# Kernel optimization log

Hardware: AMD Instinct MI355X
Metric: run time of the kernel (lower is better)

Reference implementation:

```python
import jax, jax.numpy as jnp
import numpy as np

N = 100000   # nodes
E = 600000   # edges
G = 4096     # graphs in batch
D_IN = 73
D_E = 101
D = 128      # latent_dim
BN_EPS = 1e-5


def _bn(h, gamma, beta):
    # BatchNorm1d in training mode: batch statistics (biased variance)
    m = h.mean(axis=0)
    v = h.var(axis=0)
    return (h - m) * jax.lax.rsqrt(v + BN_EPS) * gamma + beta


def setup_inputs() -> dict:
    key = jax.random.key(0)
    ks = jax.random.split(key, 24)
    inp = {
        "x": jax.random.normal(ks[0], (N, D_IN), jnp.float32),
        "edge_attr": jax.random.normal(ks[1], (E, D_E), jnp.float32),
        "src": jax.random.randint(ks[2], (E,), 0, N, jnp.int32),
        "dst": jax.random.randint(ks[3], (E,), 0, N, jnp.int32),
        "batch": jnp.sort(jax.random.randint(ks[4], (N,), 0, G, jnp.int32)),
        # node embedding Linear(73 -> 128)
        "W_emb": jax.random.normal(ks[5], (D_IN, D), jnp.float32) / np.sqrt(D_IN),
        "b_emb": jnp.zeros((D,), jnp.float32),
    }
    k = 6
    for i in range(2):
        inp[f"We{i}"] = jax.random.normal(ks[k], (D_E, D), jnp.float32) / np.sqrt(D_E); k += 1
        inp[f"be{i}"] = jnp.zeros((D,), jnp.float32)
        inp[f"W1_{i}"] = jax.random.normal(ks[k], (D, 2 * D), jnp.float32) / np.sqrt(D); k += 1
        inp[f"b1_{i}"] = jnp.zeros((2 * D,), jnp.float32)
        inp[f"g1_{i}"] = jnp.ones((2 * D,), jnp.float32)
        inp[f"bb1_{i}"] = jnp.zeros((2 * D,), jnp.float32)
        inp[f"W2_{i}"] = jax.random.normal(ks[k], (2 * D, D), jnp.float32) / np.sqrt(2 * D); k += 1
        inp[f"b2_{i}"] = jnp.zeros((D,), jnp.float32)
        inp[f"go_{i}"] = jnp.ones((D,), jnp.float32)
        inp[f"bo_{i}"] = jnp.zeros((D,), jnp.float32)
    return inp


def _forward(x, edge_attr, src, dst, batch,
             W_emb, b_emb,
             We0, be0, W1_0, b1_0, g1_0, bb1_0, W2_0, b2_0, go_0, bo_0,
             We1, be1, W1_1, b1_1, g1_1, bb1_1, W2_1, b2_1, go_1, bo_1):
    layers = [
        (We0, be0, W1_0, b1_0, g1_0, bb1_0, W2_0, b2_0, go_0, bo_0),
        (We1, be1, W1_1, b1_1, g1_1, bb1_1, W2_1, b2_1, go_1, bo_1),
    ]
    h = x @ W_emb + b_emb  # [N, D]
    n_layers = len(layers)
    for i, (We, be, W1, b1, g1, bb1, W2, b2, go, bo) in enumerate(layers):
        e = edge_attr @ We + be                         # [E, D]
        msg = jax.nn.relu(h[src] + e)                   # gather + add + ReLU
        agg = jax.ops.segment_sum(msg, dst, num_segments=N)  # scatter-sum
        z = h + agg                                     # (1 + eps) * x_i + aggr, eps = 0
        z = jax.nn.relu(_bn(z @ W1 + b1, g1, bb1))      # MLP: Linear -> BN -> ReLU
        h = _bn(z @ W2 + b2, go, bo)                    # Linear -> outer BN
        if i != n_layers - 1:
            h = jax.nn.relu(h)
        # dropout p=0 -> identity
    # global mean pool over graphs
    sums = jax.ops.segment_sum(h, batch, num_segments=G)            # [G, D]
    counts = jax.ops.segment_sum(jnp.ones((h.shape[0],), h.dtype), batch, num_segments=G)
    return sums / jnp.maximum(counts, 1.0)[:, None]


def reference(x, edge_attr, src, dst, batch,
              W_emb, b_emb,
              We0, be0, W1_0, b1_0, g1_0, bb1_0, W2_0, b2_0, go_0, bo_0,
              We1, be1, W1_1, b1_1, g1_1, bb1_1, W2_1, b2_1, go_1, bo_1):
    return _forward(x, edge_attr, src, dst, batch, W_emb, b_emb,
                    We0, be0, W1_0, b1_0, g1_0, bb1_0, W2_0, b2_0, go_0, bo_0,
                    We1, be1, W1_1, b1_1, g1_1, bb1_1, W2_1, b2_1, go_1, bo_1)
```

## Files before the change

kernel.cpp:

```cpp
#include <hip/hip_runtime.h>
#include <cstddef>

#define NN  100000
#define NE  600000
#define NG  4096
#define DIN 73
#define DE  101
#define DD  128
#define DD2 256
#define NP  100096
#define EP  600064

typedef unsigned int uint;
typedef unsigned short ushort;
typedef __attribute__((ext_vector_type(8))) short bf16x8;
typedef __attribute__((ext_vector_type(4))) float f32x4;

__device__ __forceinline__ void fadd_atomic(float* p, float v) { unsafeAtomicAdd(p, v); }

__device__ __forceinline__ ushort f2bf(float f) {
    uint u = __float_as_uint(f);
    uint r = (u + 0x7fffu + ((u >> 16) & 1u)) >> 16;
    return (ushort)r;
}
__device__ __forceinline__ float bf2f(ushort u) { return __uint_as_float(((uint)u) << 16); }


__global__ void hist_kernel(const int* __restrict__ dst, int* __restrict__ deg) {
    int e = blockIdx.x * blockDim.x + threadIdx.x;
    if (e < NE) atomicAdd(&deg[dst[e]], 1);
}

__global__ __launch_bounds__(256) void scan_chunk_kernel(
    const int* __restrict__ deg, int* __restrict__ offs, int* __restrict__ csums)
{
    const int b = blockIdx.x, t = threadIdx.x;
    const int base = b * 1024 + t * 4;
    int v[4];
    #pragma unroll
    for (int i = 0; i < 4; ++i) v[i] = (base + i < NN) ? deg[base + i] : 0;
    int tsum = v[0] + v[1] + v[2] + v[3];
    const int lane = t & 63, w = t >> 6;
    int x = tsum;
    #pragma unroll
    for (int d = 1; d < 64; d <<= 1) {
        int y = __shfl_up(x, d, 64);
        if (lane >= d) x += y;
    }
    __shared__ int wsum[4];
    if (lane == 63) wsum[w] = x;
    __syncthreads();
    int woff = 0;
    for (int i = 0; i < w; ++i) woff += wsum[i];
    int run = woff + x - tsum;
    #pragma unroll
    for (int i = 0; i < 4; ++i) {
        if (base + i < NN) offs[base + i] = run;
        run += v[i];
    }
    if (t == 255) csums[b] = woff + x;
}

__global__ void scan_tops_kernel(int* __restrict__ csums, int* __restrict__ offs, int nchunks) {
    if (threadIdx.x == 0 && blockIdx.x == 0) {
        int run = 0;
        for (int i = 0; i < nchunks; ++i) { int c = csums[i]; csums[i] = run; run += c; }
        offs[NN] = run;
    }
}

__global__ void scan_add_kernel(int* __restrict__ offs, const int* __restrict__ csums) {
    int i = blockIdx.x * blockDim.x + threadIdx.x;
    if (i < NN) offs[i] += csums[i >> 10];
}

__global__ void scatter_kernel(const int* __restrict__ dst, const int* __restrict__ src,
                               const int* __restrict__ offs, int* __restrict__ cursor,
                               int* __restrict__ eperm, int* __restrict__ srcp)
{
    int e = blockIdx.x * blockDim.x + threadIdx.x;
    if (e >= NE) return;
    int d = dst[e];
    int pos = offs[d] + atomicAdd(&cursor[d], 1);
    eperm[e] = pos;
    srcp[pos] = src[e];
}

__global__ void gstart_kernel(const int* __restrict__ batch, int* __restrict__ gstart) {
    int n = blockIdx.x * blockDim.x + threadIdx.x;
    if (n > NN) return;
    if (n == NN) {
        for (int g = batch[NN - 1] + 1; g <= NG; ++g) gstart[g] = NN;
        return;
    }
    int b = batch[n];
    int pb = (n == 0) ? -1 : batch[n - 1];
    for (int g = pb + 1; g <= b; ++g) gstart[g] = n;
}


__global__ __launch_bounds__(256) void cvt_ea_kernel(const float* __restrict__ ea,
                                                     ushort* __restrict__ eab)
{
    const int t = threadIdx.x;
    const int r = blockIdx.x * 8 + (t >> 5);
    if (r >= EP) return;
    const int c = (t & 31) * 4;
    ushort4 o = {0, 0, 0, 0};
    if (r < NE) {
        o.x = (c + 0 < DE) ? f2bf(ea[(size_t)r * DE + c + 0]) : (ushort)0;
        o.y = (c + 1 < DE) ? f2bf(ea[(size_t)r * DE + c + 1]) : (ushort)0;
        o.z = (c + 2 < DE) ? f2bf(ea[(size_t)r * DE + c + 2]) : (ushort)0;
        o.w = (c + 3 < DE) ? f2bf(ea[(size_t)r * DE + c + 3]) : (ushort)0;
    }
    *(ushort4*)&eab[(size_t)r * 128 + c] = o;
}

__global__ void cvt_wt_kernel(const float* __restrict__ in, ushort* __restrict__ out,
                              int Kin, int Nn, int Kp)
{
    const int n = blockIdx.x;
    for (int k = threadIdx.x; k < Kp; k += blockDim.x)
        out[(size_t)n * Kp + k] = (k < Kin) ? f2bf(in[(size_t)k * Nn + n]) : (ushort)0;
}

template<int K>
__device__ __forceinline__ void mma_core(const ushort* __restrict__ Wt,
                                         const ushort* __restrict__ X,
                                         int n0, int m0, f32x4 acc[4][8])
{
    const int lane = threadIdx.x & 63;
    const int l15 = lane & 15, grp = lane >> 4;
    const size_t aoff = (size_t)(n0 + l15) * K + grp * 8;
    const size_t boff = (size_t)(m0 + l15) * K + grp * 8;
    #pragma unroll
    for (int kk = 0; kk < K / 32; ++kk) {
        bf16x8 a[8], b[4];
        #pragma unroll
        for (int nf = 0; nf < 8; ++nf)
            a[nf] = *(const bf16x8*)(Wt + aoff + (size_t)nf * 16 * K + kk * 32);
        #pragma unroll
        for (int mf = 0; mf < 4; ++mf)
            b[mf] = *(const bf16x8*)(X + boff + (size_t)mf * 16 * K + kk * 32);
        #pragma unroll
        for (int mf = 0; mf < 4; ++mf)
            #pragma unroll
            for (int nf = 0; nf < 8; ++nf)
                acc[mf][nf] = __builtin_amdgcn_mfma_f32_16x16x32_bf16(a[nf], b[mf], acc[mf][nf], 0, 0, 0);
    }
}

__device__ __forceinline__ void acc_zero(f32x4 acc[4][8]) {
    #pragma unroll
    for (int i = 0; i < 4; ++i)
        #pragma unroll
        for (int j = 0; j < 8; ++j)
            acc[i][j] = (f32x4){0.f, 0.f, 0.f, 0.f};
}

__global__ __launch_bounds__(256) void edge_gemm_kernel(
    const ushort* __restrict__ eab, const ushort* __restrict__ Wt,
    const float* __restrict__ be, const int* __restrict__ eperm,
    ushort* __restrict__ ecsr)
{
    const int e0 = blockIdx.x * 256 + (threadIdx.x >> 6) * 64;
    const int lane = threadIdx.x & 63, l15 = lane & 15, grp = lane >> 4;
    int pos[4];
    #pragma unroll
    for (int mf = 0; mf < 4; ++mf) {
        const int e = e0 + mf * 16 + l15;
        pos[mf] = (e < NE) ? eperm[e] : -1;
    }
    f32x4 acc[4][8];
    acc_zero(acc);
    mma_core<128>(Wt, eab, 0, e0, acc);
    float4 bev[8];
    #pragma unroll
    for (int nf = 0; nf < 8; ++nf) bev[nf] = *(const float4*)&be[nf * 16 + grp * 4];
    #pragma unroll
    for (int mf = 0; mf < 4; ++mf) {
        if (pos[mf] < 0) continue;
        ushort* rp = &ecsr[(size_t)pos[mf] * 128];
        #pragma unroll
        for (int nf = 0; nf < 8; ++nf) {
            const int nb = nf * 16 + grp * 4;
            ushort4 o;
            o.x = f2bf(acc[mf][nf][0] + bev[nf].x);
            o.y = f2bf(acc[mf][nf][1] + bev[nf].y);
            o.z = f2bf(acc[mf][nf][2] + bev[nf].z);
            o.w = f2bf(acc[mf][nf][3] + bev[nf].w);
            *(ushort4*)&rp[nb] = o;
        }
    }
}

__global__ __launch_bounds__(256) void agg_kernel(
    const int* __restrict__ offs, const int* __restrict__ srcp,
    const ushort* __restrict__ ecsr, const ushort* __restrict__ hb,
    ushort* __restrict__ zb)
{
    const int n = blockIdx.x * 4 + (threadIdx.x >> 6);
    if (n >= NN) return;
    const int lane = threadIdx.x & 63;
    const int s = offs[n], t = offs[n + 1];
    float a0 = 0.f, a1 = 0.f;
    for (int i = s; i < t; ++i) {
        const int sp = srcp[i];
        const uint ev = *(const uint*)&ecsr[(size_t)i * 128 + lane * 2];
        const uint hv = *(const uint*)&hb[(size_t)sp * 128 + lane * 2];
        a0 += fmaxf(__uint_as_float(ev << 16) + __uint_as_float(hv << 16), 0.f);
        a1 += fmaxf(__uint_as_float(ev & 0xffff0000u) + __uint_as_float(hv & 0xffff0000u), 0.f);
    }
    const uint hh = *(const uint*)&hb[(size_t)n * 128 + lane * 2];
    ushort2 o;
    o.x = f2bf(__uint_as_float(hh << 16) + a0);
    o.y = f2bf(__uint_as_float(hh & 0xffff0000u) + a1);
    *(ushort2*)&zb[(size_t)n * 128 + lane * 2] = o;
}

__global__ __launch_bounds__(256) void mlp1_gemm_kernel(
    const ushort* __restrict__ z, const ushort* __restrict__ Wt,
    const float* __restrict__ bias, ushort* __restrict__ y)
{
    f32x4 acc[4][8];
    acc_zero(acc);
    const int m0 = blockIdx.x * 256 + (threadIdx.x >> 6) * 64;
    const int n0 = blockIdx.y * 128;
    mma_core<128>(Wt, z, n0, m0, acc);
    const int lane = threadIdx.x & 63, l15 = lane & 15, grp = lane >> 4;
    #pragma unroll
    for (int nf = 0; nf < 8; ++nf) {
        const int nb = n0 + nf * 16 + grp * 4;
        const float4 bv = *(const float4*)&bias[nb];
        #pragma unroll
        for (int mf = 0; mf < 4; ++mf) {
            const size_t m = m0 + mf * 16 + l15;
            ushort4 o;
            o.x = f2bf(acc[mf][nf][0] + bv.x);
            o.y = f2bf(acc[mf][nf][1] + bv.y);
            o.z = f2bf(acc[mf][nf][2] + bv.z);
            o.w = f2bf(acc[mf][nf][3] + bv.w);
            *(ushort4*)&y[m * 256 + nb] = o;
        }
    }
}

__global__ __launch_bounds__(256) void mlp2_gemm_kernel(
    const ushort* __restrict__ y1, const ushort* __restrict__ Wt,
    const float* __restrict__ bias, ushort* __restrict__ y2)
{
    f32x4 acc[4][8];
    acc_zero(acc);
    const int m0 = blockIdx.x * 256 + (threadIdx.x >> 6) * 64;
    mma_core<256>(Wt, y1, 0, m0, acc);
    const int lane = threadIdx.x & 63, l15 = lane & 15, grp = lane >> 4;
    #pragma unroll
    for (int nf = 0; nf < 8; ++nf) {
        const int nb = nf * 16 + grp * 4;
        const float4 bv = *(const float4*)&bias[nb];
        #pragma unroll
        for (int mf = 0; mf < 4; ++mf) {
            const size_t m = m0 + mf * 16 + l15;
            ushort4 o;
            o.x = f2bf(acc[mf][nf][0] + bv.x);
            o.y = f2bf(acc[mf][nf][1] + bv.y);
            o.z = f2bf(acc[mf][nf][2] + bv.z);
            o.w = f2bf(acc[mf][nf][3] + bv.w);
            *(ushort4*)&y2[m * 128 + nb] = o;
        }
    }
}


__global__ __launch_bounds__(128) void embed_kernel(
    const float* __restrict__ x, const float* __restrict__ W,
    const float* __restrict__ b, ushort* __restrict__ hb)
{
    __shared__ float xs[4][DIN];
    const int n0 = blockIdx.x * 4;
    const int d  = threadIdx.x;
    for (int idx = d; idx < 4 * DIN; idx += 128) {
        int r = idx / DIN, c = idx - r * DIN;
        xs[r][c] = x[(size_t)n0 * DIN + idx];
    }
    __syncthreads();
    float bb = b[d];
    float a0 = bb, a1 = bb, a2 = bb, a3 = bb;
    for (int k = 0; k < DIN; ++k) {
        float w = W[k * DD + d];
        a0 = fmaf(xs[0][k], w, a0);
        a1 = fmaf(xs[1][k], w, a1);
        a2 = fmaf(xs[2][k], w, a2);
        a3 = fmaf(xs[3][k], w, a3);
    }
    hb[(size_t)(n0 + 0) * DD + d] = f2bf(a0);
    hb[(size_t)(n0 + 1) * DD + d] = f2bf(a1);
    hb[(size_t)(n0 + 2) * DD + d] = f2bf(a2);
    hb[(size_t)(n0 + 3) * DD + d] = f2bf(a3);
}

__global__ __launch_bounds__(256) void colstats256_kernel(
    const ushort* __restrict__ y, float* __restrict__ s, float* __restrict__ q)
{
    const int t = threadIdx.x;
    const int cs = (t & 63) * 4, rg = t >> 6;
    const int r0 = blockIdx.x * 256;
    float ps0 = 0, ps1 = 0, ps2 = 0, ps3 = 0, pq0 = 0, pq1 = 0, pq2 = 0, pq3 = 0;
    for (int i = rg; i < 256; i += 4) {
        const int r = r0 + i;
        if (r >= NN) break;
        ushort4 u = *(const ushort4*)&y[(size_t)r * 256 + cs];
        float f0 = bf2f(u.x), f1 = bf2f(u.y), f2v = bf2f(u.z), f3 = bf2f(u.w);
        ps0 += f0; pq0 += f0 * f0;
        ps1 += f1; pq1 += f1 * f1;
        ps2 += f2v; pq2 += f2v * f2v;
        ps3 += f3; pq3 += f3 * f3;
    }
    __shared__ float SS[4][256], SQ[4][256];
    SS[rg][cs + 0] = ps0; SS[rg][cs + 1] = ps1; SS[rg][cs + 2] = ps2; SS[rg][cs + 3] = ps3;
    SQ[rg][cs + 0] = pq0; SQ[rg][cs + 1] = pq1; SQ[rg][cs + 2] = pq2; SQ[rg][cs + 3] = pq3;
    __syncthreads();
    if (rg == 0) {
        #pragma unroll
        for (int j = 0; j < 4; ++j) {
            const int c = cs + j;
            fadd_atomic(&s[c], SS[0][c] + SS[1][c] + SS[2][c] + SS[3][c]);
            fadd_atomic(&q[c], SQ[0][c] + SQ[1][c] + SQ[2][c] + SQ[3][c]);
        }
    }
}

__global__ __launch_bounds__(256) void colstats128b_kernel(
    const ushort* __restrict__ y, float* __restrict__ s, float* __restrict__ q)
{
    const int t = threadIdx.x;
    const int cs = (t & 31) * 4, rg = t >> 5;
    const int r0 = blockIdx.x * 256;
    float ps0 = 0, ps1 = 0, ps2 = 0, ps3 = 0, pq0 = 0, pq1 = 0, pq2 = 0, pq3 = 0;
    for (int i = rg; i < 256; i += 8) {
        const int r = r0 + i;
        if (r >= NN) break;
        ushort4 u = *(const ushort4*)&y[(size_t)r * 128 + cs];
        float f0 = bf2f(u.x), f1 = bf2f(u.y), f2v = bf2f(u.z), f3 = bf2f(u.w);
        ps0 += f0; pq0 += f0 * f0;
        ps1 += f1; pq1 += f1 * f1;
        ps2 += f2v; pq2 += f2v * f2v;
        ps3 += f3; pq3 += f3 * f3;
    }
    __shared__ float SS[8][128], SQ[8][128];
    SS[rg][cs + 0] = ps0; SS[rg][cs + 1] = ps1; SS[rg][cs + 2] = ps2; SS[rg][cs + 3] = ps3;
    SQ[rg][cs + 0] = pq0; SQ[rg][cs + 1] = pq1; SQ[rg][cs + 2] = pq2; SQ[rg][cs + 3] = pq3;
    __syncthreads();
    if (rg == 0) {
        #pragma unroll
        for (int j = 0; j < 4; ++j) {
            const int c = cs + j;
            float sv = 0, qv = 0;
            #pragma unroll
            for (int g = 0; g < 8; ++g) { sv += SS[g][c]; qv += SQ[g][c]; }
            fadd_atomic(&s[c], sv);
            fadd_atomic(&q[c], qv);
        }
    }
}

__global__ void finalize_kernel(const float* __restrict__ s, const float* __restrict__ sq,
                                const float* __restrict__ g, const float* __restrict__ bb,
                                float* __restrict__ a, float* __restrict__ c,
                                int dim, float invN)
{
    int d = blockIdx.x * blockDim.x + threadIdx.x;
    if (d >= dim) return;
    float m  = s[d] * invN;
    float v  = sq[d] * invN - m * m;
    float rs = rsqrtf(v + 1e-5f);
    float ai = g[d] * rs;
    a[d] = ai;
    c[d] = bb[d] - m * ai;
}

__global__ void bnrelu_bf_kernel(ushort* __restrict__ y, const float* __restrict__ a,
                                 const float* __restrict__ c)
{
    int i = blockIdx.x * blockDim.x + threadIdx.x;
    const int stride = gridDim.x * blockDim.x;
    for (; i < NN * 64; i += stride) {
        const int cb = (i & 63) * 4;
        ushort4 u = *(const ushort4*)&y[(size_t)i * 4];
        const float4 av = *(const float4*)&a[cb];
        const float4 cv = *(const float4*)&c[cb];
        ushort4 o;
        o.x = f2bf(fmaxf(fmaf(bf2f(u.x), av.x, cv.x), 0.f));
        o.y = f2bf(fmaxf(fmaf(bf2f(u.y), av.y, cv.y), 0.f));
        o.z = f2bf(fmaxf(fmaf(bf2f(u.z), av.z, cv.z), 0.f));
        o.w = f2bf(fmaxf(fmaf(bf2f(u.w), av.w, cv.w), 0.f));
        *(ushort4*)&y[(size_t)i * 4] = o;
    }
}

__global__ void bnrelu_hb_kernel(ushort* __restrict__ hb, const float* __restrict__ a,
                                 const float* __restrict__ c)
{
    int i = blockIdx.x * blockDim.x + threadIdx.x;
    const int stride = gridDim.x * blockDim.x;
    for (; i < NN * 32; i += stride) {
        const int cb = (i & 31) * 4;
        ushort4 u = *(const ushort4*)&hb[(size_t)i * 4];
        const float4 av = *(const float4*)&a[cb];
        const float4 cv = *(const float4*)&c[cb];
        ushort4 o;
        o.x = f2bf(fmaxf(fmaf(bf2f(u.x), av.x, cv.x), 0.f));
        o.y = f2bf(fmaxf(fmaf(bf2f(u.y), av.y, cv.y), 0.f));
        o.z = f2bf(fmaxf(fmaf(bf2f(u.z), av.z, cv.z), 0.f));
        o.w = f2bf(fmaxf(fmaf(bf2f(u.w), av.w, cv.w), 0.f));
        *(ushort4*)&hb[(size_t)i * 4] = o;
    }
}

__global__ __launch_bounds__(256) void pool_kernel(
    const ushort* __restrict__ hb, const float* __restrict__ a2, const float* __restrict__ c2,
    const int* __restrict__ gstart, float* __restrict__ out)
{
    const int g = blockIdx.x * 4 + (threadIdx.x >> 6);
    if (g >= NG) return;
    const int lane = threadIdx.x & 63;
    const int s = gstart[g], t = gstart[g + 1];
    float a0 = 0.f, a1 = 0.f;
    for (int n = s; n < t; ++n) {
        const uint v = *(const uint*)&hb[(size_t)n * 128 + lane * 2];
        a0 += __uint_as_float(v << 16);
        a1 += __uint_as_float(v & 0xffff0000u);
    }
    const int d0 = lane * 2;
    float2 o;
    if (t > s) {
        const float inv = 1.0f / (float)(t - s);
        o.x = fmaf(a2[d0 + 0], a0 * inv, c2[d0 + 0]);
        o.y = fmaf(a2[d0 + 1], a1 * inv, c2[d0 + 1]);
    } else {
        o.x = 0.f; o.y = 0.f;
    }
    *(float2*)&out[(size_t)g * 128 + d0] = o;
}


extern "C" void kernel_launch(void* const* d_in, const int* in_sizes, int n_in,
                              void* d_out, int out_size, void* d_ws, size_t ws_size,
                              hipStream_t stream)
{
    (void)in_sizes; (void)n_in; (void)out_size; (void)ws_size;
    const float* x     = (const float*)d_in[0];
    const float* ea    = (const float*)d_in[1];
    const int*   src   = (const int*)d_in[2];
    const int*   dst   = (const int*)d_in[3];
    const int*   batch = (const int*)d_in[4];
    const float* W_emb = (const float*)d_in[5];
    const float* b_emb = (const float*)d_in[6];

    char* ws = (char*)d_ws;
    auto alloc = [&](size_t bytes) { void* p = ws; ws += (bytes + 255) & ~(size_t)255; return p; };

    ushort* hb  = (ushort*)alloc((size_t)NP * 128 * 2);
    ushort* zb  = (ushort*)alloc((size_t)NP * 128 * 2);
    ushort* eab = (ushort*)alloc((size_t)EP * 128 * 2);
    ushort* big = (ushort*)alloc((size_t)EP * 128 * 2);
    ushort* ecsr = big;
    ushort* y1b  = big;
    int* deg    = (int*)alloc((size_t)NN * 4);
    int* offs   = (int*)alloc((size_t)(NN + 1) * 4);
    int* eperm  = (int*)alloc((size_t)NE * 4);
    int* srcp   = (int*)alloc((size_t)NE * 4);
    int* csums  = (int*)alloc(128 * 4);
    int* gstart = (int*)alloc((size_t)(NG + 1) * 4);
    ushort* Wet[2], *W1t[2], *W2t[2];
    for (int l = 0; l < 2; ++l) {
        Wet[l] = (ushort*)alloc(128 * 128 * 2);
        W1t[l] = (ushort*)alloc(256 * 128 * 2);
        W2t[l] = (ushort*)alloc(128 * 256 * 2);
    }
    float* st = (float*)alloc(2048 * 4);
    float* s1 = st,        *sq1 = st + 256, *a1 = st + 512,  *c1 = st + 768;
    float* s2 = st + 1024, *sq2 = st + 1152, *a2 = st + 1280, *c2 = st + 1408;
    float* out = (float*)d_out;

    const int NCHUNK = (NN + 1023) / 1024;

    hipMemsetAsync(deg, 0, (size_t)NN * 4, stream);
    hist_kernel<<<(NE + 255) / 256, 256, 0, stream>>>(dst, deg);
    scan_chunk_kernel<<<NCHUNK, 256, 0, stream>>>(deg, offs, csums);
    scan_tops_kernel<<<1, 1, 0, stream>>>(csums, offs, NCHUNK);
    scan_add_kernel<<<(NN + 255) / 256, 256, 0, stream>>>(offs, csums);
    hipMemsetAsync(deg, 0, (size_t)NN * 4, stream);
    scatter_kernel<<<(NE + 255) / 256, 256, 0, stream>>>(dst, src, offs, deg, eperm, srcp);
    gstart_kernel<<<(NN + 256) / 256, 256, 0, stream>>>(batch, gstart);

    cvt_ea_kernel<<<EP / 8, 256, 0, stream>>>(ea, eab);
    for (int l = 0; l < 2; ++l) {
        const float* const* L = (const float* const*)(d_in + 7 + l * 10);
        cvt_wt_kernel<<<128, 128, 0, stream>>>(L[0], Wet[l], 101, 128, 128);
        cvt_wt_kernel<<<256, 128, 0, stream>>>(L[2], W1t[l], 128, 256, 128);
        cvt_wt_kernel<<<128, 128, 0, stream>>>(L[6], W2t[l], 256, 128, 256);
    }

    embed_kernel<<<NN / 4, 128, 0, stream>>>(x, W_emb, b_emb, hb);

    for (int layer = 0; layer < 2; ++layer) {
        const float* const* L = (const float* const*)(d_in + 7 + layer * 10);
        const float* be  = L[1];
        const float* b1  = L[3];
        const float* g1  = L[4]; const float* bb1 = L[5];
        const float* b2  = L[7];
        const float* go  = L[8]; const float* bo  = L[9];

        edge_gemm_kernel<<<EP / 256, 256, 0, stream>>>(eab, Wet[layer], be, eperm, ecsr);
        agg_kernel<<<NN / 4, 256, 0, stream>>>(offs, srcp, ecsr, hb, zb);

        hipMemsetAsync(s1, 0, 512 * sizeof(float), stream);
        hipMemsetAsync(s2, 0, 256 * sizeof(float), stream);

        mlp1_gemm_kernel<<<dim3(NP / 256, 2), 256, 0, stream>>>(zb, W1t[layer], b1, y1b);
        colstats256_kernel<<<NP / 256, 256, 0, stream>>>(y1b, s1, sq1);
        finalize_kernel<<<1, 256, 0, stream>>>(s1, sq1, g1, bb1, a1, c1, 256, 1.0f / NN);
        bnrelu_bf_kernel<<<2048, 256, 0, stream>>>(y1b, a1, c1);
        mlp2_gemm_kernel<<<NP / 256, 256, 0, stream>>>(y1b, W2t[layer], b2, hb);
        colstats128b_kernel<<<NP / 256, 256, 0, stream>>>(hb, s2, sq2);
        finalize_kernel<<<1, 128, 0, stream>>>(s2, sq2, go, bo, a2, c2, 128, 1.0f / NN);

        if (layer == 0) {
            bnrelu_hb_kernel<<<2048, 256, 0, stream>>>(hb, a2, c2);
        } else {
            pool_kernel<<<NG / 4, 256, 0, stream>>>(hb, a2, c2, gstart, out);
        }
    }
}
```

Measured before the change: 1.149 ms.

## Pre-permute edge features to CSR order and make GEMMs persistent with register-resident weights

Edge attributes are now scattered into CSR (dst-sorted) order during the bf16 conversion, with an appended ones column. The edge bias is folded into the transposed weight matrix through that column. As a result the edge GEMM writes its output rows contiguously instead of scattering them through eperm. The edge, MLP1 and MLP2 GEMMs become persistent grid-stride kernels: each wave keeps its weight slice in registers and splits the N dimension across waves, with launch_bounds set for two blocks per CU. The cost is higher register pressure, and the bf16 conversion now does a scattered 256-byte row write.

```diff
diff --git a/kernel.cpp b/kernel.cpp
--- a/kernel.cpp
+++ b/kernel.cpp
@@ -100,98 +100,220 @@
 
 
 __global__ __launch_bounds__(256) void cvt_ea_kernel(const float* __restrict__ ea,
-                                                     ushort* __restrict__ eab)
+                                                     const int* __restrict__ eperm,
+                                                     ushort* __restrict__ eabc)
 {
     const int t = threadIdx.x;
     const int r = blockIdx.x * 8 + (t >> 5);
-    if (r >= EP) return;
+    if (r >= NE) return;
+    const int pos = eperm[r];
     const int c = (t & 31) * 4;
-    ushort4 o = {0, 0, 0, 0};
-    if (r < NE) {
-        o.x = (c + 0 < DE) ? f2bf(ea[(size_t)r * DE + c + 0]) : (ushort)0;
-        o.y = (c + 1 < DE) ? f2bf(ea[(size_t)r * DE + c + 1]) : (ushort)0;
-        o.z = (c + 2 < DE) ? f2bf(ea[(size_t)r * DE + c + 2]) : (ushort)0;
-        o.w = (c + 3 < DE) ? f2bf(ea[(size_t)r * DE + c + 3]) : (ushort)0;
-    }
-    *(ushort4*)&eab[(size_t)r * 128 + c] = o;
+    ushort4 o;
+    #pragma unroll
+    for (int i = 0; i < 4; ++i) {
+        const int col = c + i;
+        float v = (col < DE) ? ea[(size_t)r * DE + col] : ((col == DE) ? 1.0f : 0.0f);
+        ((ushort*)&o)[i] = f2bf(v);
+    }
+    *(ushort4*)&eabc[(size_t)pos * 128 + c] = o;
 }
 
 __global__ void cvt_wt_kernel(const float* __restrict__ in, ushort* __restrict__ out,
-                              int Kin, int Nn, int Kp)
+                              int Kin, int Nn, int Kp, const float* __restrict__ bias)
 {
     const int n = blockIdx.x;
-    for (int k = threadIdx.x; k < Kp; k += blockDim.x)
-        out[(size_t)n * Kp + k] = (k < Kin) ? f2bf(in[(size_t)k * Nn + n]) : (ushort)0;
-}
-
-template<int K>
-__device__ __forceinline__ void mma_core(const ushort* __restrict__ Wt,
-                                         const ushort* __restrict__ X,
-                                         int n0, int m0, f32x4 acc[4][8])
-{
-    const int lane = threadIdx.x & 63;
-    const int l15 = lane & 15, grp = lane >> 4;
-    const size_t aoff = (size_t)(n0 + l15) * K + grp * 8;
-    const size_t boff = (size_t)(m0 + l15) * K + grp * 8;
-    #pragma unroll
-    for (int kk = 0; kk < K / 32; ++kk) {
-        bf16x8 a[8], b[4];
-        #pragma unroll
-        for (int nf = 0; nf < 8; ++nf)
-            a[nf] = *(const bf16x8*)(Wt + aoff + (size_t)nf * 16 * K + kk * 32);
-        #pragma unroll
-        for (int mf = 0; mf < 4; ++mf)
-            b[mf] = *(const bf16x8*)(X + boff + (size_t)mf * 16 * K + kk * 32);
-        #pragma unroll
-        for (int mf = 0; mf < 4; ++mf)
-            #pragma unroll
-            for (int nf = 0; nf < 8; ++nf)
-                acc[mf][nf] = __builtin_amdgcn_mfma_f32_16x16x32_bf16(a[nf], b[mf], acc[mf][nf], 0, 0, 0);
-    }
-}
-
-__device__ __forceinline__ void acc_zero(f32x4 acc[4][8]) {
-    #pragma unroll
-    for (int i = 0; i < 4; ++i)
-        #pragma unroll
-        for (int j = 0; j < 8; ++j)
-            acc[i][j] = (f32x4){0.f, 0.f, 0.f, 0.f};
-}
-
-__global__ __launch_bounds__(256) void edge_gemm_kernel(
+    for (int k = threadIdx.x; k < Kp; k += blockDim.x) {
+        float v = 0.0f;
+        if (k < Kin) v = in[(size_t)k * Nn + n];
+        else if (k == Kin && bias) v = bias[n];
+        out[(size_t)n * Kp + k] = f2bf(v);
+    }
+}
+
+
+__global__ __launch_bounds__(256, 2) void edge_gemm_kernel(
     const ushort* __restrict__ eab, const ushort* __restrict__ Wt,
-    const float* __restrict__ be, const int* __restrict__ eperm,
     ushort* __restrict__ ecsr)
 {
-    const int e0 = blockIdx.x * 256 + (threadIdx.x >> 6) * 64;
+    const int wid = threadIdx.x >> 6;
+    const int msub = wid >> 1, nsl = wid & 1;
     const int lane = threadIdx.x & 63, l15 = lane & 15, grp = lane >> 4;
-    int pos[4];
-    #pragma unroll
-    for (int mf = 0; mf < 4; ++mf) {
-        const int e = e0 + mf * 16 + l15;
-        pos[mf] = (e < NE) ? eperm[e] : -1;
-    }
-    f32x4 acc[4][8];
-    acc_zero(acc);
-    mma_core<128>(Wt, eab, 0, e0, acc);
-    float4 bev[8];
-    #pragma unroll
-    for (int nf = 0; nf < 8; ++nf) bev[nf] = *(const float4*)&be[nf * 16 + grp * 4];
-    #pragma unroll
-    for (int mf = 0; mf < 4; ++mf) {
-        if (pos[mf] < 0) continue;
-        ushort* rp = &ecsr[(size_t)pos[mf] * 128];
-        #pragma unroll
-        for (int nf = 0; nf < 8; ++nf) {
-            const int nb = nf * 16 + grp * 4;
-            ushort4 o;
-            o.x = f2bf(acc[mf][nf][0] + bev[nf].x);
-            o.y = f2bf(acc[mf][nf][1] + bev[nf].y);
-            o.z = f2bf(acc[mf][nf][2] + bev[nf].z);
-            o.w = f2bf(acc[mf][nf][3] + bev[nf].w);
-            *(ushort4*)&rp[nb] = o;
-        }
-    }
+    const int n0 = nsl * 64;
+    bf16x8 A[4][4];
+    #pragma unroll
+    for (int nf = 0; nf < 4; ++nf)
+        #pragma unroll
+        for (int kk = 0; kk < 4; ++kk)
+            A[nf][kk] = *(const bf16x8*)(Wt + (size_t)(n0 + nf * 16 + l15) * 128 + kk * 32 + grp * 8);
+
+    const int ntiles = EP / 128;
+    for (int t = blockIdx.x; t < ntiles; t += gridDim.x) {
+        const int m0 = t * 128 + msub * 64;
+        f32x4 acc[4][4];
+        #pragma unroll
+        for (int i = 0; i < 4; ++i)
+            #pragma unroll
+            for (int j = 0; j < 4; ++j) acc[i][j] = (f32x4){0.f, 0.f, 0.f, 0.f};
+        #pragma unroll
+        for (int kk = 0; kk < 4; ++kk) {
+            bf16x8 b[4];
+            #pragma unroll
+            for (int mf = 0; mf < 4; ++mf)
+                b[mf] = *(const bf16x8*)(eab + (size_t)(m0 + mf * 16 + l15) * 128 + kk * 32 + grp * 8);
+            #pragma unroll
+            for (int mf = 0; mf < 4; ++mf)
+                #pragma unroll
+                for (int nf = 0; nf < 4; ++nf)
+                    acc[mf][nf] = __builtin_amdgcn_mfma_f32_16x16x32_bf16(A[nf][kk], b[mf], acc[mf][nf], 0, 0, 0);
+        }
+        #pragma unroll
+        for (int mf = 0; mf < 4; ++mf) {
+            ushort* rp = &ecsr[(size_t)(m0 + mf * 16 + l15) * 128 + n0];
+            #pragma unroll
+            for (int nf = 0; nf < 4; ++nf) {
+                ushort4 o;
+                o.x = f2bf(acc[mf][nf][0]);
+                o.y = f2bf(acc[mf][nf][1]);
+                o.z = f2bf(acc[mf][nf][2]);
+                o.w = f2bf(acc[mf][nf][3]);
+                *(ushort4*)&rp[nf * 16 + grp * 4] = o;
+            }
+        }
+    }
+}
+
+__global__ __launch_bounds__(256, 2) void mlp1_gemm_kernel(
+    const ushort* __restrict__ z, const ushort* __restrict__ Wt,
+    const float* __restrict__ bias, ushort* __restrict__ y)
+{
+    const int n0 = (threadIdx.x >> 6) * 64;
+    const int lane = threadIdx.x & 63, l15 = lane & 15, grp = lane >> 4;
+    bf16x8 A[4][4];
+    #pragma unroll
+    for (int nf = 0; nf < 4; ++nf)
+        #pragma unroll
+        for (int kk = 0; kk < 4; ++kk)
+            A[nf][kk] = *(const bf16x8*)(Wt + (size_t)(n0 + nf * 16 + l15) * 128 + kk * 32 + grp * 8);
+    float4 bv[4];
+    #pragma unroll
+    for (int nf = 0; nf < 4; ++nf) bv[nf] = *(const float4*)&bias[n0 + nf * 16 + grp * 4];
+
+    const int ntiles = NP / 64;
+    for (int t = blockIdx.x; t < ntiles; t += gridDim.x) {
+        const int m0 = t * 64;
+        f32x4 acc[4][4];
+        #pragma unroll
+        for (int i = 0; i < 4; ++i)
+            #pragma unroll
+            for (int j = 0; j < 4; ++j) acc[i][j] = (f32x4){0.f, 0.f, 0.f, 0.f};
+        #pragma unroll
+        for (int kk = 0; kk < 4; ++kk) {
+            bf16x8 b[4];
+            #pragma unroll
+            for (int mf = 0; mf < 4; ++mf)
+                b[mf] = *(const bf16x8*)(z + (size_t)(m0 + mf * 16 + l15) * 128 + kk * 32 + grp * 8);
+            #pragma unroll
+            for (int mf = 0; mf < 4; ++mf)
+                #pragma unroll
+                for (int nf = 0; nf < 4; ++nf)
+                    acc[mf][nf] = __builtin_amdgcn_mfma_f32_16x16x32_bf16(A[nf][kk], b[mf], acc[mf][nf], 0, 0, 0);
+        }
+        #pragma unroll
+        for (int mf = 0; mf < 4; ++mf) {
+            ushort* rp = &y[(size_t)(m0 + mf * 16 + l15) * 256 + n0];
+            #pragma unroll
+            for (int nf = 0; nf < 4; ++nf) {
+                ushort4 o;
+                o.x = f2bf(acc[mf][nf][0] + bv[nf].x);
+                o.y = f2bf(acc[mf][nf][1] + bv[nf].y);
+                o.z = f2bf(acc[mf][nf][2] + bv[nf].z);
+                o.w = f2bf(acc[mf][nf][3] + bv[nf].w);
+                *(ushort4*)&rp[nf * 16 + grp * 4] = o;
+            }
+        }
+    }
+}
+
+__global__ __launch_bounds__(256, 2) void mlp2_gemm_kernel(
+    const ushort* __restrict__ y1, const ushort* __restrict__ Wt,
+    const float* __restrict__ bias, ushort* __restrict__ y2)
+{
+    const int wid = threadIdx.x >> 6;
+    const int msub = wid >> 1, nsl = wid & 1;
+    const int lane = threadIdx.x & 63, l15 = lane & 15, grp = lane >> 4;
+    const int n0 = nsl * 64;
+    bf16x8 A[4][8];
+    #pragma unroll
+    for (int nf = 0; nf < 4; ++nf)
+        #pragma unroll
+        for (int kk = 0; kk < 8; ++kk)
+            A[nf][kk] = *(const bf16x8*)(Wt + (size_t)(n0 + nf * 16 + l15) * 256 + kk * 32 + grp * 8);
+    float4 bv[4];
+    #pragma unroll
+    for (int nf = 0; nf < 4; ++nf) bv[nf] = *(const float4*)&bias[n0 + nf * 16 + grp * 4];
+
+    const int ntiles = NP / 128;
+    for (int t = blockIdx.x; t < ntiles; t += gridDim.x) {
+        const int m0 = t * 128 + msub * 64;
+        f32x4 acc[4][4];
+        #pragma unroll
+        for (int i = 0; i < 4; ++i)
+            #pragma unroll
+            for (int j = 0; j < 4; ++j) acc[i][j] = (f32x4){0.f, 0.f, 0.f, 0.f};
+        #pragma unroll
+        for (int kk = 0; kk < 8; ++kk) {
+            bf16x8 b[4];
+            #pragma unroll
+            for (int mf = 0; mf < 4; ++mf)
+                b[mf] = *(const bf16x8*)(y1 + (size_t)(m0 + mf * 16 + l15) * 256 + kk * 32 + grp * 8);
+            #pragma unroll
+            for (int mf = 0; mf < 4; ++mf)
+                #pragma unroll
+                for (int nf = 0; nf < 4; ++nf)
+                    acc[mf][nf] = __builtin_amdgcn_mfma_f32_16x16x32_bf16(A[nf][kk], b[mf], acc[mf][nf], 0, 0, 0);
+        }
+        #pragma unroll
+        for (int mf = 0; mf < 4; ++mf) {
+            ushort* rp = &y2[(size_t)(m0 + mf * 16 + l15) * 128 + n0];
+            #pragma unroll
+            for (int nf = 0; nf < 4; ++nf) {
+                ushort4 o;
+                o.x = f2bf(acc[mf][nf][0] + bv[nf].x);
+                o.y = f2bf(acc[mf][nf][1] + bv[nf].y);
+                o.z = f2bf(acc[mf][nf][2] + bv[nf].z);
+                o.w = f2bf(acc[mf][nf][3] + bv[nf].w);
+                *(ushort4*)&rp[nf * 16 + grp * 4] = o;
+            }
+        }
+    }
+}
+
+
+__global__ __launch_bounds__(128) void embed_kernel(
+    const float* __restrict__ x, const float* __restrict__ W,
+    const float* __restrict__ b, ushort* __restrict__ hb)
+{
+    __shared__ float xs[4][DIN];
+    const int n0 = blockIdx.x * 4;
+    const int d  = threadIdx.x;
+    for (int idx = d; idx < 4 * DIN; idx += 128) {
+        int r = idx / DIN, c = idx - r * DIN;
+        xs[r][c] = x[(size_t)n0 * DIN + idx];
+    }
+    __syncthreads();
+    float bb = b[d];
+    float a0 = bb, a1 = bb, a2 = bb, a3 = bb;
+    for (int k = 0; k < DIN; ++k) {
+        float w = W[k * DD + d];
+        a0 = fmaf(xs[0][k], w, a0);
+        a1 = fmaf(xs[1][k], w, a1);
+        a2 = fmaf(xs[2][k], w, a2);
+        a3 = fmaf(xs[3][k], w, a3);
+    }
+    hb[(size_t)(n0 + 0) * DD + d] = f2bf(a0);
+    hb[(size_t)(n0 + 1) * DD + d] = f2bf(a1);
+    hb[(size_t)(n0 + 2) * DD + d] = f2bf(a2);
+    hb[(size_t)(n0 + 3) * DD + d] = f2bf(a3);
 }
 
 __global__ __launch_bounds__(256) void agg_kernel(
@@ -216,87 +338,6 @@
     o.x = f2bf(__uint_as_float(hh << 16) + a0);
     o.y = f2bf(__uint_as_float(hh & 0xffff0000u) + a1);
     *(ushort2*)&zb[(size_t)n * 128 + lane * 2] = o;
-}
-
-__global__ __launch_bounds__(256) void mlp1_gemm_kernel(
-    const ushort* __restrict__ z, const ushort* __restrict__ Wt,
-    const float* __restrict__ bias, ushort* __restrict__ y)
-{
-    f32x4 acc[4][8];
-    acc_zero(acc);
-    const int m0 = blockIdx.x * 256 + (threadIdx.x >> 6) * 64;
-    const int n0 = blockIdx.y * 128;
-    mma_core<128>(Wt, z, n0, m0, acc);
-    const int lane = threadIdx.x & 63, l15 = lane & 15, grp = lane >> 4;
-    #pragma unroll
-    for (int nf = 0; nf < 8; ++nf) {
-        const int nb = n0 + nf * 16 + grp * 4;
-        const float4 bv = *(const float4*)&bias[nb];
-        #pragma unroll
-        for (int mf = 0; mf < 4; ++mf) {
-            const size_t m = m0 + mf * 16 + l15;
-            ushort4 o;
-            o.x = f2bf(acc[mf][nf][0] + bv.x);
-            o.y = f2bf(acc[mf][nf][1] + bv.y);
-            o.z = f2bf(acc[mf][nf][2] + bv.z);
-            o.w = f2bf(acc[mf][nf][3] + bv.w);
-            *(ushort4*)&y[m * 256 + nb] = o;
-        }
-    }
-}
-
-__global__ __launch_bounds__(256) void mlp2_gemm_kernel(
-    const ushort* __restrict__ y1, const ushort* __restrict__ Wt,
-    const float* __restrict__ bias, ushort* __restrict__ y2)
-{
-    f32x4 acc[4][8];
-    acc_zero(acc);
-    const int m0 = blockIdx.x * 256 + (threadIdx.x >> 6) * 64;
-    mma_core<256>(Wt, y1, 0, m0, acc);
-    const int lane = threadIdx.x & 63, l15 = lane & 15, grp = lane >> 4;
-    #pragma unroll
-    for (int nf = 0; nf < 8; ++nf) {
-        const int nb = nf * 16 + grp * 4;
-        const float4 bv = *(const float4*)&bias[nb];
-        #pragma unroll
-        for (int mf = 0; mf < 4; ++mf) {
-            const size_t m = m0 + mf * 16 + l15;
-            ushort4 o;
-            o.x = f2bf(acc[mf][nf][0] + bv.x);
-            o.y = f2bf(acc[mf][nf][1] + bv.y);
-            o.z = f2bf(acc[mf][nf][2] + bv.z);
-            o.w = f2bf(acc[mf][nf][3] + bv.w);
-            *(ushort4*)&y2[m * 128 + nb] = o;
-        }
-    }
-}
-
-
-__global__ __launch_bounds__(128) void embed_kernel(
-    const float* __restrict__ x, const float* __restrict__ W,
-    const float* __restrict__ b, ushort* __restrict__ hb)
-{
-    __shared__ float xs[4][DIN];
-    const int n0 = blockIdx.x * 4;
-    const int d  = threadIdx.x;
-    for (int idx = d; idx < 4 * DIN; idx += 128) {
-        int r = idx / DIN, c = idx - r * DIN;
-        xs[r][c] = x[(size_t)n0 * DIN + idx];
-    }
-    __syncthreads();
-    float bb = b[d];
-    float a0 = bb, a1 = bb, a2 = bb, a3 = bb;
-    for (int k = 0; k < DIN; ++k) {
-        float w = W[k * DD + d];
-        a0 = fmaf(xs[0][k], w, a0);
-        a1 = fmaf(xs[1][k], w, a1);
-        a2 = fmaf(xs[2][k], w, a2);
-        a3 = fmaf(xs[3][k], w, a3);
-    }
-    hb[(size_t)(n0 + 0) * DD + d] = f2bf(a0);
-    hb[(size_t)(n0 + 1) * DD + d] = f2bf(a1);
-    hb[(size_t)(n0 + 2) * DD + d] = f2bf(a2);
-    hb[(size_t)(n0 + 3) * DD + d] = f2bf(a3);
 }
 
 __global__ __launch_bounds__(256) void colstats256_kernel(
@@ -460,10 +501,10 @@
     char* ws = (char*)d_ws;
     auto alloc = [&](size_t bytes) { void* p = ws; ws += (bytes + 255) & ~(size_t)255; return p; };
 
-    ushort* hb  = (ushort*)alloc((size_t)NP * 128 * 2);
-    ushort* zb  = (ushort*)alloc((size_t)NP * 128 * 2);
-    ushort* eab = (ushort*)alloc((size_t)EP * 128 * 2);
-    ushort* big = (ushort*)alloc((size_t)EP * 128 * 2);
+    ushort* hb   = (ushort*)alloc((size_t)NP * 128 * 2);
+    ushort* zb   = (ushort*)alloc((size_t)NP * 128 * 2);
+    ushort* eabc = (ushort*)alloc((size_t)EP * 128 * 2);
+    ushort* big  = (ushort*)alloc((size_t)EP * 128 * 2);
     ushort* ecsr = big;
     ushort* y1b  = big;
     int* deg    = (int*)alloc((size_t)NN * 4);
@@ -494,36 +535,35 @@
     scatter_kernel<<<(NE + 255) / 256, 256, 0, stream>>>(dst, src, offs, deg, eperm, srcp);
     gstart_kernel<<<(NN + 256) / 256, 256, 0, stream>>>(batch, gstart);
 
-    cvt_ea_kernel<<<EP / 8, 256, 0, stream>>>(ea, eab);
+    cvt_ea_kernel<<<(NE + 7) / 8, 256, 0, stream>>>(ea, eperm, eabc);
     for (int l = 0; l < 2; ++l) {
         const float* const* L = (const float* const*)(d_in + 7 + l * 10);
-        cvt_wt_kernel<<<128, 128, 0, stream>>>(L[0], Wet[l], 101, 128, 128);
-        cvt_wt_kernel<<<256, 128, 0, stream>>>(L[2], W1t[l], 128, 256, 128);
-        cvt_wt_kernel<<<128, 128, 0, stream>>>(L[6], W2t[l], 256, 128, 256);
+        cvt_wt_kernel<<<128, 128, 0, stream>>>(L[0], Wet[l], 101, 128, 128, L[1]);
+        cvt_wt_kernel<<<256, 128, 0, stream>>>(L[2], W1t[l], 128, 256, 128, nullptr);
+        cvt_wt_kernel<<<128, 128, 0, stream>>>(L[6], W2t[l], 256, 128, 256, nullptr);
     }
 
     embed_kernel<<<NN / 4, 128, 0, stream>>>(x, W_emb, b_emb, hb);
 
     for (int layer = 0; layer < 2; ++layer) {
         const float* const* L = (const float* const*)(d_in + 7 + layer * 10);
-        const float* be  = L[1];
         const float* b1  = L[3];
         const float* g1  = L[4]; const float* bb1 = L[5];
         const float* b2  = L[7];
         const float* go  = L[8]; const float* bo  = L[9];
 
-        edge_gemm_kernel<<<EP / 256, 256, 0, stream>>>(eab, Wet[layer], be, eperm, ecsr);
+        edge_gemm_kernel<<<1172, 256, 0, stream>>>(eabc, Wet[layer], ecsr);
         agg_kernel<<<NN / 4, 256, 0, stream>>>(offs, srcp, ecsr, hb, zb);
 
         hipMemsetAsync(s1, 0, 512 * sizeof(float), stream);
         hipMemsetAsync(s2, 0, 256 * sizeof(float), stream);
 
-        mlp1_gemm_kernel<<<dim3(NP / 256, 2), 256, 0, stream>>>(zb, W1t[layer], b1, y1b);
-        colstats256_kernel<<<NP / 256, 256, 0, stream>>>(y1b, s1, sq1);
+        mlp1_gemm_kernel<<<782, 256, 0, stream>>>(zb, W1t[layer], b1, y1b);
+        colstats256_kernel<<<NP / 256 + 1, 256, 0, stream>>>(y1b, s1, sq1);
         finalize_kernel<<<1, 256, 0, stream>>>(s1, sq1, g1, bb1, a1, c1, 256, 1.0f / NN);
         bnrelu_bf_kernel<<<2048, 256, 0, stream>>>(y1b, a1, c1);
-        mlp2_gemm_kernel<<<NP / 256, 256, 0, stream>>>(y1b, W2t[layer], b2, hb);
-        colstats128b_kernel<<<NP / 256, 256, 0, stream>>>(hb, s2, sq2);
+        mlp2_gemm_kernel<<<391, 256, 0, stream>>>(y1b, W2t[layer], b2, hb);
+        colstats128b_kernel<<<NP / 256 + 1, 256, 0, stream>>>(hb, s2, sq2);
         finalize_kernel<<<1, 128, 0, stream>>>(s2, sq2, go, bo, a2, c2, 128, 1.0f / NN);
 
         if (layer == 0) {
```

New measurement: 1.055 ms. 8.2% less time.
